# Kernel optimization log

Measured on AMD Instinct MI355X. Metric: run time of the kernel, lower is better.

The kernel has to match this reference:

```python
import jax, jax.numpy as jnp
import numpy as np

N_NODES = 100000
N_EDGES = 1000000
D_FEAT = 64


def setup_inputs() -> dict:
    key = jax.random.key(0)
    k1, k2, k3 = jax.random.split(key, 3)
    features = jax.random.normal(k1, (N_NODES, D_FEAT), dtype=jnp.float32)
    src = jax.random.randint(k2, (N_EDGES,), 0, N_NODES, dtype=jnp.int64)
    dst = jax.random.randint(k3, (N_EDGES,), 0, N_NODES, dtype=jnp.int64)
    return {"features": features, "src": src, "dst": dst}


def reference(features, src, dst):
    # DGL update_all(copy_u('h','m'), sum('m','h')):
    # out[v] = sum_{(u,v) in E} features[u]
    msgs = features[src]  # [E, D] gather of source node features
    h = jax.ops.segment_sum(msgs, dst, num_segments=N_NODES)  # [N, D] scatter-add
    return h
```

## Files before the change

kernel.cpp:

```cpp
#include <hip/hip_runtime.h>


#define N_NODES   100000
#define N_EDGES   1000000
#define D_FEAT    64
#define NPB       128
#define NPB_SHIFT 7
#define NB        782
#define PAD       32
#define EPB       8192
#define CH        2048

typedef unsigned int uint;
typedef unsigned short ushort;

__device__ inline ushort f2bf(float f) {
    uint u = __float_as_uint(f);
    uint lsb = (u >> 16) & 1u;
    u += 0x7fffu + lsb;
    return (ushort)(u >> 16);
}

__global__ __launch_bounds__(256) void convert_kernel(const float* __restrict__ feat,
                                                      ushort* __restrict__ bfeat,
                                                      int* __restrict__ gcounts,
                                                      int n4, int nzero) {
    int i = blockIdx.x * blockDim.x + threadIdx.x;
    if (i < nzero) gcounts[i] = 0;
    if (i < n4) {
        float4 v = ((const float4*)feat)[i];
        ushort4 o;
        o.x = f2bf(v.x); o.y = f2bf(v.y); o.z = f2bf(v.z); o.w = f2bf(v.w);
        ((ushort4*)bfeat)[i] = o;
    }
}

__global__ __launch_bounds__(512) void hist_kernel(const int* __restrict__ dst,
                                                   int* __restrict__ gcounts, int n) {
    __shared__ int cnt[NB];
    for (int i = threadIdx.x; i < NB; i += 512) cnt[i] = 0;
    __syncthreads();
    int base = blockIdx.x * EPB + threadIdx.x * 4;
#pragma unroll
    for (int step = 0; step < 4; ++step) {
        int idx = base + step * 2048;
        if (idx < n) {
            int4 d = *reinterpret_cast<const int4*>(dst + idx);
            atomicAdd(&cnt[d.x >> NPB_SHIFT], 1);
            atomicAdd(&cnt[d.y >> NPB_SHIFT], 1);
            atomicAdd(&cnt[d.z >> NPB_SHIFT], 1);
            atomicAdd(&cnt[d.w >> NPB_SHIFT], 1);
        }
    }
    __syncthreads();
    for (int b = threadIdx.x; b < NB; b += 512)
        if (cnt[b]) atomicAdd(&gcounts[b * PAD], cnt[b]);
}

__global__ __launch_bounds__(1024) void scan_kernel(const int* __restrict__ gcounts,
                                                    int* __restrict__ bases,
                                                    int* __restrict__ gcursor, int n_edges) {
    __shared__ int lds[1024];
    int t = threadIdx.x;
    int v = (t < NB) ? gcounts[t * PAD] : 0;
    lds[t] = v;
    __syncthreads();
    for (int off = 1; off < 1024; off <<= 1) {
        int u = (t >= off) ? lds[t - off] : 0;
        __syncthreads();
        lds[t] += u;
        __syncthreads();
    }
    if (t < NB) { int b = lds[t] - v; bases[t] = b; gcursor[t * PAD] = b; }
    if (t == 0) bases[NB] = n_edges;
}

__global__ __launch_bounds__(512) void partition_kernel(const int* __restrict__ src,
                                                        const int* __restrict__ dst,
                                                        int* __restrict__ gcursor,
                                                        int* __restrict__ pairs, int n) {
    __shared__ int cnt[NB];
    __shared__ int lbase[NB];
    for (int i = threadIdx.x; i < NB; i += 512) cnt[i] = 0;
    __syncthreads();

    int base = blockIdx.x * EPB + threadIdx.x * 4;
    int4 s[4], d[4];
    bool valid[4];
#pragma unroll
    for (int step = 0; step < 4; ++step) {
        int idx = base + step * 2048;
        valid[step] = (idx < n);
        if (valid[step]) {
            s[step] = *reinterpret_cast<const int4*>(src + idx);
            d[step] = *reinterpret_cast<const int4*>(dst + idx);
            atomicAdd(&cnt[d[step].x >> NPB_SHIFT], 1);
            atomicAdd(&cnt[d[step].y >> NPB_SHIFT], 1);
            atomicAdd(&cnt[d[step].z >> NPB_SHIFT], 1);
            atomicAdd(&cnt[d[step].w >> NPB_SHIFT], 1);
        }
    }
    __syncthreads();
    for (int b = threadIdx.x; b < NB; b += 512) {
        int c = cnt[b];
        lbase[b] = c ? atomicAdd(&gcursor[b * PAD], c) : 0;
    }
    __syncthreads();
    for (int b = threadIdx.x; b < NB; b += 512) cnt[b] = 0;
    __syncthreads();
#pragma unroll
    for (int step = 0; step < 4; ++step) {
        if (valid[step]) {
            int b, p;
            b = d[step].x >> NPB_SHIFT; p = atomicAdd(&cnt[b], 1); pairs[lbase[b] + p] = (s[step].x << NPB_SHIFT) | (d[step].x & (NPB - 1));
            b = d[step].y >> NPB_SHIFT; p = atomicAdd(&cnt[b], 1); pairs[lbase[b] + p] = (s[step].y << NPB_SHIFT) | (d[step].y & (NPB - 1));
            b = d[step].z >> NPB_SHIFT; p = atomicAdd(&cnt[b], 1); pairs[lbase[b] + p] = (s[step].z << NPB_SHIFT) | (d[step].z & (NPB - 1));
            b = d[step].w >> NPB_SHIFT; p = atomicAdd(&cnt[b], 1); pairs[lbase[b] + p] = (s[step].w << NPB_SHIFT) | (d[step].w & (NPB - 1));
        }
    }
}

__device__ inline float4 bf4_to_f4(uint2 v) {
    float4 r;
    r.x = __uint_as_float(v.x << 16);
    r.y = __uint_as_float(v.x & 0xffff0000u);
    r.z = __uint_as_float(v.y << 16);
    r.w = __uint_as_float(v.y & 0xffff0000u);
    return r;
}

__global__ __launch_bounds__(256) void gather16_kernel(const ushort* __restrict__ bfeat,
                                                       const int* __restrict__ bases,
                                                       const int* __restrict__ pairs,
                                                       float* __restrict__ out,
                                                       int n_nodes) {
    __shared__ int pbuf[CH];
    __shared__ int sorted[CH];
    __shared__ int deg[32];
    __shared__ int sc[32];
    __shared__ int start[33];
    __shared__ int cur[32];

    int bb = blockIdx.x >> 2;
    int q  = blockIdx.x & 3;
    int t = threadIdx.x;
    int grp = t >> 4;
    int l16 = t & 15;
    int lo = bases[bb], hi = bases[bb + 1];
    int node0 = bb * NPB + q * 32;

    bool first = true;
    for (int c = lo; c < hi || first; c += CH) {
        int n = hi - c;
        if (n > CH) n = CH;
        if (n < 0) n = 0;

        if (t < 32) deg[t] = 0;
        __syncthreads();
        for (int i = t; i < n; i += 256) {
            int p = pairs[c + i];
            pbuf[i] = p;
            int r = p & (NPB - 1);
            if ((r >> 5) == q) atomicAdd(&deg[r & 31], 1);
        }
        __syncthreads();
        if (t < 32) sc[t] = deg[t];
        __syncthreads();
        for (int off = 1; off < 32; off <<= 1) {
            int u = (t < 32 && t >= off) ? sc[t - off] : 0;
            __syncthreads();
            if (t < 32) sc[t] += u;
            __syncthreads();
        }
        if (t < 32) { start[t + 1] = sc[t]; cur[t] = sc[t] - deg[t]; }
        if (t == 0) start[0] = 0;
        __syncthreads();
        for (int i = t; i < n; i += 256) {
            int p = pbuf[i];
            int r = p & (NPB - 1);
            if ((r >> 5) == q) {
                int pos = atomicAdd(&cur[r & 31], 1);
                sorted[pos] = p >> NPB_SHIFT;
            }
        }
        __syncthreads();

        for (int r = grp; r < 32; r += 16) {
            int s0 = start[r], e0 = start[r + 1];
            float4 a0 = {0.f, 0.f, 0.f, 0.f}, a1 = a0, a2 = a0, a3 = a0;
            int i = s0;
            for (; i + 4 <= e0; i += 4) {
                int n0 = sorted[i], n1 = sorted[i + 1];
                int n2 = sorted[i + 2], n3 = sorted[i + 3];
                uint2 w0 = *reinterpret_cast<const uint2*>(bfeat + (size_t)n0 * D_FEAT + l16 * 4);
                uint2 w1 = *reinterpret_cast<const uint2*>(bfeat + (size_t)n1 * D_FEAT + l16 * 4);
                uint2 w2 = *reinterpret_cast<const uint2*>(bfeat + (size_t)n2 * D_FEAT + l16 * 4);
                uint2 w3 = *reinterpret_cast<const uint2*>(bfeat + (size_t)n3 * D_FEAT + l16 * 4);
                float4 v0 = bf4_to_f4(w0), v1 = bf4_to_f4(w1);
                float4 v2 = bf4_to_f4(w2), v3 = bf4_to_f4(w3);
                a0.x += v0.x; a0.y += v0.y; a0.z += v0.z; a0.w += v0.w;
                a1.x += v1.x; a1.y += v1.y; a1.z += v1.z; a1.w += v1.w;
                a2.x += v2.x; a2.y += v2.y; a2.z += v2.z; a2.w += v2.w;
                a3.x += v3.x; a3.y += v3.y; a3.z += v3.z; a3.w += v3.w;
            }
            for (; i < e0; ++i) {
                uint2 w = *reinterpret_cast<const uint2*>(bfeat + (size_t)sorted[i] * D_FEAT + l16 * 4);
                float4 v = bf4_to_f4(w);
                a0.x += v.x; a0.y += v.y; a0.z += v.z; a0.w += v.w;
            }
            float4 acc;
            acc.x = (a0.x + a1.x) + (a2.x + a3.x);
            acc.y = (a0.y + a1.y) + (a2.y + a3.y);
            acc.z = (a0.z + a1.z) + (a2.z + a3.z);
            acc.w = (a0.w + a1.w) + (a2.w + a3.w);

            int node = node0 + r;
            if (node < n_nodes) {
                float* o = out + (size_t)node * D_FEAT + l16 * 4;
                if (first) {
                    *reinterpret_cast<float4*>(o) = acc;
                } else {
                    atomicAdd(o + 0, acc.x); atomicAdd(o + 1, acc.y);
                    atomicAdd(o + 2, acc.z); atomicAdd(o + 3, acc.w);
                }
            }
        }
        first = false;
        __syncthreads();
    }
}

__global__ __launch_bounds__(256) void gather32_kernel(const float* __restrict__ feat,
                                                       const int* __restrict__ bases,
                                                       const int* __restrict__ pairs,
                                                       float* __restrict__ out,
                                                       int n_nodes) {
    __shared__ int pbuf[CH];
    __shared__ int sorted[CH];
    __shared__ int deg[32];
    __shared__ int sc[32];
    __shared__ int start[33];
    __shared__ int cur[32];

    int bb = blockIdx.x >> 2;
    int q  = blockIdx.x & 3;
    int t = threadIdx.x;
    int grp = t >> 4, l16 = t & 15;
    int lo = bases[bb], hi = bases[bb + 1];
    int node0 = bb * NPB + q * 32;

    bool first = true;
    for (int c = lo; c < hi || first; c += CH) {
        int n = hi - c;
        if (n > CH) n = CH;
        if (n < 0) n = 0;

        if (t < 32) deg[t] = 0;
        __syncthreads();
        for (int i = t; i < n; i += 256) {
            int p = pairs[c + i];
            pbuf[i] = p;
            int r = p & (NPB - 1);
            if ((r >> 5) == q) atomicAdd(&deg[r & 31], 1);
        }
        __syncthreads();
        if (t < 32) sc[t] = deg[t];
        __syncthreads();
        for (int off = 1; off < 32; off <<= 1) {
            int u = (t < 32 && t >= off) ? sc[t - off] : 0;
            __syncthreads();
            if (t < 32) sc[t] += u;
            __syncthreads();
        }
        if (t < 32) { start[t + 1] = sc[t]; cur[t] = sc[t] - deg[t]; }
        if (t == 0) start[0] = 0;
        __syncthreads();
        for (int i = t; i < n; i += 256) {
            int p = pbuf[i];
            int r = p & (NPB - 1);
            if ((r >> 5) == q) {
                int pos = atomicAdd(&cur[r & 31], 1);
                sorted[pos] = p >> NPB_SHIFT;
            }
        }
        __syncthreads();

        for (int r = grp; r < 32; r += 16) {
            int s0 = start[r], e0 = start[r + 1];
            float4 a0 = {0.f, 0.f, 0.f, 0.f};
            for (int i = s0; i < e0; ++i) {
                const float4 v = *reinterpret_cast<const float4*>(feat + (size_t)sorted[i] * D_FEAT + l16 * 4);
                a0.x += v.x; a0.y += v.y; a0.z += v.z; a0.w += v.w;
            }
            int node = node0 + r;
            if (node < n_nodes) {
                float* o = out + (size_t)node * D_FEAT + l16 * 4;
                if (first) *reinterpret_cast<float4*>(o) = a0;
                else {
                    atomicAdd(o + 0, a0.x); atomicAdd(o + 1, a0.y);
                    atomicAdd(o + 2, a0.z); atomicAdd(o + 3, a0.w);
                }
            }
        }
        first = false;
        __syncthreads();
    }
}

__global__ void zero_ints_kernel(int* __restrict__ p, int n) {
    int i = blockIdx.x * blockDim.x + threadIdx.x;
    if (i < n) p[i] = 0;
}

extern "C" void kernel_launch(void* const* d_in, const int* in_sizes, int n_in,
                              void* d_out, int out_size, void* d_ws, size_t ws_size,
                              hipStream_t stream) {
    const float* feat = (const float*)d_in[0];
    const int*   src  = (const int*)d_in[1];
    const int*   dst  = (const int*)d_in[2];
    float*       out  = (float*)d_out;

    const int n_edges = in_sizes[1];

    int* gcounts = (int*)d_ws;
    int* gcursor = gcounts + NB * PAD;
    int* bases   = gcursor + NB * PAD;
    int* pairs   = bases + NB + 1;
    size_t int_off = (size_t)(NB * PAD * 2 + NB + 1) + (size_t)n_edges;
    size_t bf_off  = (int_off * 4 + 7) & ~(size_t)7;
    ushort* bfeat  = (ushort*)((char*)d_ws + bf_off);
    size_t need = bf_off + (size_t)N_NODES * D_FEAT * 2;

    const int nzero = NB * PAD;
    const int pblocks = (n_edges + EPB - 1) / EPB;

    if (ws_size >= need) {
        int n4 = N_NODES * D_FEAT / 4;
        convert_kernel<<<(n4 + 255) / 256, 256, 0, stream>>>(feat, bfeat, gcounts, n4, nzero);
        hist_kernel<<<pblocks, 512, 0, stream>>>(dst, gcounts, n_edges);
        scan_kernel<<<1, 1024, 0, stream>>>(gcounts, bases, gcursor, n_edges);
        partition_kernel<<<pblocks, 512, 0, stream>>>(src, dst, gcursor, pairs, n_edges);
        gather16_kernel<<<NB * 4, 256, 0, stream>>>(bfeat, bases, pairs, out, N_NODES);
    } else {
        zero_ints_kernel<<<(nzero + 255) / 256, 256, 0, stream>>>(gcounts, nzero);
        hist_kernel<<<pblocks, 512, 0, stream>>>(dst, gcounts, n_edges);
        scan_kernel<<<1, 1024, 0, stream>>>(gcounts, bases, gcursor, n_edges);
        partition_kernel<<<pblocks, 512, 0, stream>>>(src, dst, gcursor, pairs, n_edges);
        gather32_kernel<<<NB * 4, 256, 0, stream>>>(feat, bases, pairs, out, N_NODES);
    }
}
```

Baseline: 75.69 us.

## Fuse convert with histogram and use per-block count table for partition

Merges the bf16 conversion and the per-bucket histogram into one launch, and writes per-block bucket counts to a table instead of doing global atomics. The scan kernel does a serial column prefix over that table, so partition gets deterministic per-block offsets and no longer recounts buckets or takes global atomic cursors. This removes one launch, the zeroing step, the duplicate counting pass and the global atomic contention. In exchange the scan kernel loops serially over 123 blocks per bucket, and partition output order becomes deterministic per block.

```diff
diff --git a/kernel.cpp b/kernel.cpp
--- a/kernel.cpp
+++ b/kernel.cpp
@@ -7,7 +7,6 @@
 #define NPB       128
 #define NPB_SHIFT 7
 #define NB        782
-#define PAD       32
 #define EPB       8192
 #define CH        2048
 
@@ -21,30 +20,34 @@
     return (ushort)(u >> 16);
 }
 
-__global__ __launch_bounds__(256) void convert_kernel(const float* __restrict__ feat,
-                                                      ushort* __restrict__ bfeat,
-                                                      int* __restrict__ gcounts,
-                                                      int n4, int nzero) {
-    int i = blockIdx.x * blockDim.x + threadIdx.x;
-    if (i < nzero) gcounts[i] = 0;
-    if (i < n4) {
-        float4 v = ((const float4*)feat)[i];
-        ushort4 o;
-        o.x = f2bf(v.x); o.y = f2bf(v.y); o.z = f2bf(v.z); o.w = f2bf(v.w);
-        ((ushort4*)bfeat)[i] = o;
-    }
-}
-
-__global__ __launch_bounds__(512) void hist_kernel(const int* __restrict__ dst,
-                                                   int* __restrict__ gcounts, int n) {
+__global__ __launch_bounds__(256) void conv_hist_kernel(const float* __restrict__ feat,
+                                                        ushort* __restrict__ bfeat,
+                                                        const int* __restrict__ dst,
+                                                        int* __restrict__ cnt_table,
+                                                        int n4, int n_edges, int pblocks,
+                                                        int do_conv) {
     __shared__ int cnt[NB];
-    for (int i = threadIdx.x; i < NB; i += 512) cnt[i] = 0;
+    int t = threadIdx.x;
+
+    if (do_conv) {
+        int i = blockIdx.x * 256 + t;
+        if (i < n4) {
+            float4 v = ((const float4*)feat)[i];
+            ushort4 o;
+            o.x = f2bf(v.x); o.y = f2bf(v.y); o.z = f2bf(v.z); o.w = f2bf(v.w);
+            ((ushort4*)bfeat)[i] = o;
+        }
+    }
+
+    if (blockIdx.x >= (uint)pblocks) return;
+
+    for (int i = t; i < NB; i += 256) cnt[i] = 0;
     __syncthreads();
-    int base = blockIdx.x * EPB + threadIdx.x * 4;
+    int base = blockIdx.x * EPB + t * 4;
 #pragma unroll
-    for (int step = 0; step < 4; ++step) {
-        int idx = base + step * 2048;
-        if (idx < n) {
+    for (int step = 0; step < 8; ++step) {
+        int idx = base + step * 1024;
+        if (idx < n_edges) {
             int4 d = *reinterpret_cast<const int4*>(dst + idx);
             atomicAdd(&cnt[d.x >> NPB_SHIFT], 1);
             atomicAdd(&cnt[d.y >> NPB_SHIFT], 1);
@@ -53,17 +56,26 @@
         }
     }
     __syncthreads();
-    for (int b = threadIdx.x; b < NB; b += 512)
-        if (cnt[b]) atomicAdd(&gcounts[b * PAD], cnt[b]);
-}
-
-__global__ __launch_bounds__(1024) void scan_kernel(const int* __restrict__ gcounts,
+    for (int b = t; b < NB; b += 256) cnt_table[blockIdx.x * NB + b] = cnt[b];
+}
+
+__global__ __launch_bounds__(1024) void scan_kernel(int* __restrict__ cnt_table,
                                                     int* __restrict__ bases,
-                                                    int* __restrict__ gcursor, int n_edges) {
+                                                    int n_edges, int pblocks) {
     __shared__ int lds[1024];
     int t = threadIdx.x;
-    int v = (t < NB) ? gcounts[t * PAD] : 0;
-    lds[t] = v;
+    int total = 0;
+    if (t < NB) {
+        int run = 0;
+        for (int pb = 0; pb < pblocks; ++pb) {
+            int idx = pb * NB + t;
+            int c = cnt_table[idx];
+            cnt_table[idx] = run;
+            run += c;
+        }
+        total = run;
+    }
+    lds[t] = total;
     __syncthreads();
     for (int off = 1; off < 1024; off <<= 1) {
         int u = (t >= off) ? lds[t - off] : 0;
@@ -71,51 +83,33 @@
         lds[t] += u;
         __syncthreads();
     }
-    if (t < NB) { int b = lds[t] - v; bases[t] = b; gcursor[t * PAD] = b; }
+    if (t < NB) bases[t] = lds[t] - total;
     if (t == 0) bases[NB] = n_edges;
 }
 
 __global__ __launch_bounds__(512) void partition_kernel(const int* __restrict__ src,
                                                         const int* __restrict__ dst,
-                                                        int* __restrict__ gcursor,
+                                                        const int* __restrict__ bases,
+                                                        const int* __restrict__ cnt_table,
                                                         int* __restrict__ pairs, int n) {
-    __shared__ int cnt[NB];
-    __shared__ int lbase[NB];
-    for (int i = threadIdx.x; i < NB; i += 512) cnt[i] = 0;
+    __shared__ int cur[NB];
+    int t = threadIdx.x;
+    for (int b = t; b < NB; b += 512)
+        cur[b] = bases[b] + cnt_table[blockIdx.x * NB + b];
     __syncthreads();
 
-    int base = blockIdx.x * EPB + threadIdx.x * 4;
-    int4 s[4], d[4];
-    bool valid[4];
+    int base = blockIdx.x * EPB + t * 4;
 #pragma unroll
     for (int step = 0; step < 4; ++step) {
         int idx = base + step * 2048;
-        valid[step] = (idx < n);
-        if (valid[step]) {
-            s[step] = *reinterpret_cast<const int4*>(src + idx);
-            d[step] = *reinterpret_cast<const int4*>(dst + idx);
-            atomicAdd(&cnt[d[step].x >> NPB_SHIFT], 1);
-            atomicAdd(&cnt[d[step].y >> NPB_SHIFT], 1);
-            atomicAdd(&cnt[d[step].z >> NPB_SHIFT], 1);
-            atomicAdd(&cnt[d[step].w >> NPB_SHIFT], 1);
-        }
-    }
-    __syncthreads();
-    for (int b = threadIdx.x; b < NB; b += 512) {
-        int c = cnt[b];
-        lbase[b] = c ? atomicAdd(&gcursor[b * PAD], c) : 0;
-    }
-    __syncthreads();
-    for (int b = threadIdx.x; b < NB; b += 512) cnt[b] = 0;
-    __syncthreads();
-#pragma unroll
-    for (int step = 0; step < 4; ++step) {
-        if (valid[step]) {
+        if (idx < n) {
+            int4 s = *reinterpret_cast<const int4*>(src + idx);
+            int4 d = *reinterpret_cast<const int4*>(dst + idx);
             int b, p;
-            b = d[step].x >> NPB_SHIFT; p = atomicAdd(&cnt[b], 1); pairs[lbase[b] + p] = (s[step].x << NPB_SHIFT) | (d[step].x & (NPB - 1));
-            b = d[step].y >> NPB_SHIFT; p = atomicAdd(&cnt[b], 1); pairs[lbase[b] + p] = (s[step].y << NPB_SHIFT) | (d[step].y & (NPB - 1));
-            b = d[step].z >> NPB_SHIFT; p = atomicAdd(&cnt[b], 1); pairs[lbase[b] + p] = (s[step].z << NPB_SHIFT) | (d[step].z & (NPB - 1));
-            b = d[step].w >> NPB_SHIFT; p = atomicAdd(&cnt[b], 1); pairs[lbase[b] + p] = (s[step].w << NPB_SHIFT) | (d[step].w & (NPB - 1));
+            b = d.x >> NPB_SHIFT; p = atomicAdd(&cur[b], 1); pairs[p] = (s.x << NPB_SHIFT) | (d.x & (NPB - 1));
+            b = d.y >> NPB_SHIFT; p = atomicAdd(&cur[b], 1); pairs[p] = (s.y << NPB_SHIFT) | (d.y & (NPB - 1));
+            b = d.z >> NPB_SHIFT; p = atomicAdd(&cur[b], 1); pairs[p] = (s.z << NPB_SHIFT) | (d.z & (NPB - 1));
+            b = d.w >> NPB_SHIFT; p = atomicAdd(&cur[b], 1); pairs[p] = (s.w << NPB_SHIFT) | (d.w & (NPB - 1));
         }
     }
 }
@@ -307,11 +301,6 @@
     }
 }
 
-__global__ void zero_ints_kernel(int* __restrict__ p, int n) {
-    int i = blockIdx.x * blockDim.x + threadIdx.x;
-    if (i < n) p[i] = 0;
-}
-
 extern "C" void kernel_launch(void* const* d_in, const int* in_sizes, int n_in,
                               void* d_out, int out_size, void* d_ws, size_t ws_size,
                               hipStream_t stream) {
@@ -321,31 +310,31 @@
     float*       out  = (float*)d_out;
 
     const int n_edges = in_sizes[1];
-
-    int* gcounts = (int*)d_ws;
-    int* gcursor = gcounts + NB * PAD;
-    int* bases   = gcursor + NB * PAD;
-    int* pairs   = bases + NB + 1;
-    size_t int_off = (size_t)(NB * PAD * 2 + NB + 1) + (size_t)n_edges;
-    size_t bf_off  = (int_off * 4 + 7) & ~(size_t)7;
+    const int pblocks = (n_edges + EPB - 1) / EPB;
+    const int n4 = N_NODES * D_FEAT / 4;
+    const int cblocks = (n4 + 255) / 256;
+
+    int* cnt_table = (int*)d_ws;
+    int* bases     = cnt_table + (size_t)pblocks * NB;
+    int* pairs     = bases + NB + 1;
+    size_t int_cnt = (size_t)pblocks * NB + (NB + 1) + (size_t)n_edges;
+    size_t bf_off  = (int_cnt * 4 + 7) & ~(size_t)7;
     ushort* bfeat  = (ushort*)((char*)d_ws + bf_off);
     size_t need = bf_off + (size_t)N_NODES * D_FEAT * 2;
 
-    const int nzero = NB * PAD;
-    const int pblocks = (n_edges + EPB - 1) / EPB;
+    int grid = (cblocks > pblocks) ? cblocks : pblocks;
 
     if (ws_size >= need) {
-        int n4 = N_NODES * D_FEAT / 4;
-        convert_kernel<<<(n4 + 255) / 256, 256, 0, stream>>>(feat, bfeat, gcounts, n4, nzero);
-        hist_kernel<<<pblocks, 512, 0, stream>>>(dst, gcounts, n_edges);
-        scan_kernel<<<1, 1024, 0, stream>>>(gcounts, bases, gcursor, n_edges);
-        partition_kernel<<<pblocks, 512, 0, stream>>>(src, dst, gcursor, pairs, n_edges);
+        conv_hist_kernel<<<grid, 256, 0, stream>>>(feat, bfeat, dst, cnt_table,
+                                                   n4, n_edges, pblocks, 1);
+        scan_kernel<<<1, 1024, 0, stream>>>(cnt_table, bases, n_edges, pblocks);
+        partition_kernel<<<pblocks, 512, 0, stream>>>(src, dst, bases, cnt_table, pairs, n_edges);
         gather16_kernel<<<NB * 4, 256, 0, stream>>>(bfeat, bases, pairs, out, N_NODES);
     } else {
-        zero_ints_kernel<<<(nzero + 255) / 256, 256, 0, stream>>>(gcounts, nzero);
-        hist_kernel<<<pblocks, 512, 0, stream>>>(dst, gcounts, n_edges);
-        scan_kernel<<<1, 1024, 0, stream>>>(gcounts, bases, gcursor, n_edges);
-        partition_kernel<<<pblocks, 512, 0, stream>>>(src, dst, gcursor, pairs, n_edges);
+        conv_hist_kernel<<<pblocks, 256, 0, stream>>>(feat, nullptr, dst, cnt_table,
+                                                      n4, n_edges, pblocks, 0);
+        scan_kernel<<<1, 1024, 0, stream>>>(cnt_table, bases, n_edges, pblocks);
+        partition_kernel<<<pblocks, 512, 0, stream>>>(src, dst, bases, cnt_table, pairs, n_edges);
         gather32_kernel<<<NB * 4, 256, 0, stream>>>(feat, bases, pairs, out, N_NODES);
     }
 }
```

Measured after the change: 93.40 us. 1.23x slower.
